# Performance work log

Measured on AMD Instinct MI355X. Metric: run time of the kernel, lower is better.

## Reference

```python
import jax, jax.numpy as jnp
import numpy as np

N_NODES = 50000
N_EDGES = 800000
D_IN = 96
HID = 96
D_OUT = 64
NUM_LAYERS = 6  # conv1 + (NUM_LAYERS-2) hidden convs + out_conv


def gcn_conv(x, W, b, src, dst, n):
    """PyG GCNConv: add self-loops, symmetric D^-1/2 (A+I) D^-1/2 normalization."""
    h = x @ W  # [n, out_dim]
    loops = jnp.arange(n, dtype=src.dtype)
    s = jnp.concatenate([src, loops])
    d = jnp.concatenate([dst, loops])
    deg = jax.ops.segment_sum(jnp.ones_like(s, dtype=h.dtype), d, num_segments=n)
    dinv = jnp.where(deg > 0, jax.lax.rsqrt(deg), 0.0)
    norm = dinv[s] * dinv[d]                 # [E+n]
    msg = h[s] * norm[:, None]               # gather + scale
    out = jax.ops.segment_sum(msg, d, num_segments=n)  # scatter-add to targets
    return out + b


def setup_inputs() -> dict:
    key = jax.random.key(0)
    ks = jax.random.split(key, 10)
    x = jax.random.normal(ks[0], (N_NODES, D_IN), dtype=jnp.float32)
    edge_index = jax.random.randint(ks[1], (2, N_EDGES), 0, N_NODES, dtype=jnp.int32)
    ricci_curvature = jax.random.normal(ks[2], (N_EDGES,), dtype=jnp.float32)
    n_hidden = NUM_LAYERS - 2
    W1 = jax.random.normal(ks[3], (D_IN, HID), dtype=jnp.float32) * 0.05
    b1 = jnp.zeros((HID,), dtype=jnp.float32)
    Ws = jax.random.normal(ks[4], (n_hidden, HID, HID), dtype=jnp.float32) * 0.05
    bs = jnp.zeros((n_hidden, HID), dtype=jnp.float32)
    Wout = jax.random.normal(ks[5], ((NUM_LAYERS - 1) * HID, D_OUT), dtype=jnp.float32) * 0.05
    bout = jnp.zeros((D_OUT,), dtype=jnp.float32)
    return {
        "x": x, "edge_index": edge_index, "percent": 70,
        "ricci_curvature": ricci_curvature,
        "W1": W1, "b1": b1, "Ws": Ws, "bs": bs, "Wout": Wout, "bout": bout,
    }


def reference(x, edge_index, percent, ricci_curvature, W1, b1, Ws, bs, Wout, bout):
    # Eval path: no sampling / dynamic reweighting, dropout is identity, no BN.
    del percent, ricci_curvature
    n = x.shape[0]
    src, dst = edge_index[0], edge_index[1]
    res = []
    h = jax.nn.relu(gcn_conv(x, W1, b1, src, dst, n))
    res.append(h)
    for i in range(Ws.shape[0]):
        h = jax.nn.relu(gcn_conv(h, Ws[i], bs[i], src, dst, n))
        res.append(h)
    x_cat = jnp.concatenate(res, axis=1)  # JK concatenation: [n, (L-1)*HID]
    out = gcn_conv(x_cat, Wout, bout, src, dst, n)
    return (out,) + tuple(res)
```

## Files before the change

kernel.cpp:

```cpp
#include <hip/hip_runtime.h>


typedef unsigned short ushortT;
typedef __attribute__((ext_vector_type(8))) short bf16x8;
typedef __attribute__((ext_vector_type(4))) float f32x4;

__device__ __forceinline__ ushortT f2b(float f) {
    union { float f; unsigned int u; } v;
    v.f = f;
    unsigned int lsb = (v.u >> 16) & 1u;
    v.u += 0x7fffu + lsb;
    return (ushortT)(v.u >> 16);
}
__device__ __forceinline__ float b2f(ushortT u) {
    union { float f; unsigned int u; } v;
    v.u = ((unsigned int)u) << 16;
    return v.f;
}

__global__ void prep_kernel(const float* __restrict__ W1, const float* __restrict__ Wsl,
                            const float* __restrict__ Wout, ushortT* __restrict__ wt1,
                            ushortT* __restrict__ wts, ushortT* __restrict__ wto,
                            int* __restrict__ degi, int n) {
    const int SQ = 96 * 96;
    const int T1 = 5 * SQ;
    const int T2 = T1 + 480 * 64;
    int i = blockIdx.x * blockDim.x + threadIdx.x;
    if (i < T1) {
        int l = i / SQ, j = i - l * SQ;
        int c = j / 96, k = j - c * 96;
        if (l == 0)
            wt1[j] = f2b(W1[k * 96 + c]);
        else
            wts[(size_t)(l - 1) * SQ + j] = f2b(Wsl[(size_t)(l - 1) * SQ + k * 96 + c]);
    } else if (i < T2) {
        int j = i - T1;
        int c = j / 480, k = j - c * 480;
        wto[j] = f2b(Wout[(size_t)k * 64 + c]);
    } else {
        int j = i - T2;
        if (j < n) degi[j] = 0;
    }
}

__global__ void count_kernel(const int* __restrict__ dst, int* __restrict__ degi, int E) {
    int e = blockIdx.x * blockDim.x + threadIdx.x;
    if (e < E) atomicAdd(&degi[dst[e]], 1);
}

__global__ void scan1(const int* __restrict__ degi, int* __restrict__ row_start,
                      int* __restrict__ partials, int n) {
    __shared__ int tmp[256];
    const int t = threadIdx.x;
    const int i = blockIdx.x * 256 + t;
    int val = (i < n) ? degi[i] : 0;
    tmp[t] = val;
    __syncthreads();
    for (int off = 1; off < 256; off <<= 1) {
        int v = (t >= off) ? tmp[t - off] : 0;
        __syncthreads();
        tmp[t] += v;
        __syncthreads();
    }
    if (i < n) row_start[i] = tmp[t] - val;
    if (t == 255) partials[blockIdx.x] = tmp[255];
}

__global__ void scan2(int* __restrict__ partials, int nb) {
    __shared__ int tmp[256];
    const int t = threadIdx.x;
    int val = (t < nb) ? partials[t] : 0;
    tmp[t] = val;
    __syncthreads();
    for (int off = 1; off < 256; off <<= 1) {
        int v = (t >= off) ? tmp[t - off] : 0;
        __syncthreads();
        tmp[t] += v;
        __syncthreads();
    }
    if (t < nb) partials[t] = tmp[t] - val;
}

__global__ void scan3(const int* __restrict__ degi, int* __restrict__ row_start,
                      const int* __restrict__ partials, float* __restrict__ dinv,
                      int n, int E) {
    const int i = blockIdx.x * 256 + threadIdx.x;
    if (i < n) {
        row_start[i] += partials[blockIdx.x];
        dinv[i] = rsqrtf((float)degi[i] + 1.0f);
    }
    if (i == 0) row_start[n] = E;
}

__global__ void fill_kernel(const int* __restrict__ src, const int* __restrict__ dst,
                            const int* __restrict__ row_start, int* __restrict__ degi,
                            int* __restrict__ col, int E) {
    int e = blockIdx.x * blockDim.x + threadIdx.x;
    if (e < E) {
        int d = dst[e];
        int pos = row_start[d] + atomicSub(&degi[d], 1) - 1;
        col[pos] = src[e];
    }
}

template <typename TIN>
__global__ __launch_bounds__(256) void gemm96_mfma(const TIN* __restrict__ X,
                                                   const ushortT* __restrict__ Wt,
                                                   const float* __restrict__ dinv,
                                                   ushortT* __restrict__ g, int n) {
    __shared__ __attribute__((aligned(16))) ushortT Xl[64][104];
    __shared__ __attribute__((aligned(16))) ushortT Wtl[96][104];
    const int tid = threadIdx.x;
    const int wave = tid >> 6, lane = tid & 63;
    const int quad = lane >> 4, m = lane & 15;
    const int row_base = blockIdx.x * 64;
    for (int i = tid; i < 96 * 24; i += 256) {
        int r = i / 24, c4 = (i % 24) * 4;
        *(ushort4*)&Wtl[r][c4] = *(const ushort4*)&Wt[r * 96 + c4];
    }
    for (int i = tid; i < 64 * 24; i += 256) {
        int r = i / 24, c4 = (i % 24) * 4;
        int grow = min(row_base + r, n - 1);
        if constexpr (sizeof(TIN) == 4) {
            float4 v = *(const float4*)&X[(size_t)grow * 96 + c4];
            ushort4 o = {f2b(v.x), f2b(v.y), f2b(v.z), f2b(v.w)};
            *(ushort4*)&Xl[r][c4] = o;
        } else {
            *(ushort4*)&Xl[r][c4] = *(const ushort4*)&X[(size_t)grow * 96 + c4];
        }
    }
    __syncthreads();
    f32x4 acc[6] = {};
#pragma unroll
    for (int ks = 0; ks < 3; ++ks) {
        bf16x8 a = *(bf16x8*)&Xl[wave * 16 + m][ks * 32 + quad * 8];
#pragma unroll
        for (int ct = 0; ct < 6; ++ct) {
            bf16x8 b = *(bf16x8*)&Wtl[ct * 16 + m][ks * 32 + quad * 8];
            acc[ct] = __builtin_amdgcn_mfma_f32_16x16x32_bf16(a, b, acc[ct], 0, 0, 0);
        }
    }
    float di[4];
    int rows[4];
#pragma unroll
    for (int r = 0; r < 4; ++r) {
        rows[r] = row_base + wave * 16 + quad * 4 + r;
        di[r] = (rows[r] < n) ? dinv[rows[r]] : 0.f;
    }
#pragma unroll
    for (int ct = 0; ct < 6; ++ct) {
        int colx = ct * 16 + m;
#pragma unroll
        for (int r = 0; r < 4; ++r)
            if (rows[r] < n) g[(size_t)rows[r] * 96 + colx] = f2b(acc[ct][r] * di[r]);
    }
}

template <typename TIN>
__global__ __launch_bounds__(256) void gemm_out_mfma(const TIN* __restrict__ hcat,
                                                     const ushortT* __restrict__ Wt,
                                                     const float* __restrict__ dinv,
                                                     ushortT* __restrict__ g, int n) {
    __shared__ __attribute__((aligned(16))) ushortT Xl[64][104];
    __shared__ __attribute__((aligned(16))) ushortT Wtl[64][104];
    const int tid = threadIdx.x;
    const int wave = tid >> 6, lane = tid & 63;
    const int quad = lane >> 4, m = lane & 15;
    const int row_base = blockIdx.x * 64;
    f32x4 acc[4] = {};
    for (int seg = 0; seg < 5; ++seg) {
        const TIN* hl = hcat + (size_t)seg * (size_t)n * 96;
        __syncthreads();
        for (int i = tid; i < 64 * 24; i += 256) {
            int r = i / 24, c4 = (i % 24) * 4;
            *(ushort4*)&Wtl[r][c4] = *(const ushort4*)&Wt[r * 480 + seg * 96 + c4];
        }
        for (int i = tid; i < 64 * 24; i += 256) {
            int r = i / 24, c4 = (i % 24) * 4;
            int grow = min(row_base + r, n - 1);
            if constexpr (sizeof(TIN) == 4) {
                float4 v = *(const float4*)&hl[(size_t)grow * 96 + c4];
                ushort4 o = {f2b(v.x), f2b(v.y), f2b(v.z), f2b(v.w)};
                *(ushort4*)&Xl[r][c4] = o;
            } else {
                *(ushort4*)&Xl[r][c4] = *(const ushort4*)&hl[(size_t)grow * 96 + c4];
            }
        }
        __syncthreads();
#pragma unroll
        for (int ks = 0; ks < 3; ++ks) {
            bf16x8 a = *(bf16x8*)&Xl[wave * 16 + m][ks * 32 + quad * 8];
#pragma unroll
            for (int ct = 0; ct < 4; ++ct) {
                bf16x8 b = *(bf16x8*)&Wtl[ct * 16 + m][ks * 32 + quad * 8];
                acc[ct] = __builtin_amdgcn_mfma_f32_16x16x32_bf16(a, b, acc[ct], 0, 0, 0);
            }
        }
    }
    float di[4];
    int rows[4];
#pragma unroll
    for (int r = 0; r < 4; ++r) {
        rows[r] = row_base + wave * 16 + quad * 4 + r;
        di[r] = (rows[r] < n) ? dinv[rows[r]] : 0.f;
    }
#pragma unroll
    for (int ct = 0; ct < 4; ++ct) {
        int colx = ct * 16 + m;
#pragma unroll
        for (int r = 0; r < 4; ++r)
            if (rows[r] < n) g[(size_t)rows[r] * 64 + colx] = f2b(acc[ct][r] * di[r]);
    }
}

template <int F, bool RELU, bool WRITE_BF16>
__global__ void agg_csr(const int* __restrict__ row_start, const int* __restrict__ col,
                        const ushortT* __restrict__ g, const float* __restrict__ dinv,
                        const float* __restrict__ b, float* __restrict__ out,
                        ushortT* __restrict__ hb, int n) {
    constexpr int NV = F / 4;
    const int lane = threadIdx.x & 63;
    const int half = lane >> 5;
    const int l32 = lane & 31;
    const int v = blockIdx.x * (blockDim.x >> 6) + (threadIdx.x >> 6);
    if (v >= n) return;
    const int e0 = row_start[v];
    const int e1 = row_start[v + 1];
    const bool act = (l32 < NV);
    const size_t fo = (size_t)l32 * 4;
    float a0 = 0.f, a1 = 0.f, a2 = 0.f, a3 = 0.f;
    float s0 = 0.f, s1 = 0.f, s2 = 0.f, s3 = 0.f;
    if (half == 0 && act) {
        ushort4 s = *(const ushort4*)&g[(size_t)v * F + fo];
        a0 = b2f(s.x); a1 = b2f(s.y); a2 = b2f(s.z); a3 = b2f(s.w);
    }
    const int total = e1 - e0;
    const int cntH = (total - half + 1) >> 1;
    const int base = e0 + half;
    const int sb = half << 5;
    int done = 0;
    while (done < cntH) {
        const int kc = min(cntH - done, 32);
        int cv = 0;
        if (l32 < kc) cv = col[base + 2 * (done + l32)];
        int j = 0;
        for (; j + 8 <= kc; j += 8) {
            int c0 = __shfl(cv, sb + j + 0);
            int c1 = __shfl(cv, sb + j + 1);
            int c2 = __shfl(cv, sb + j + 2);
            int c3 = __shfl(cv, sb + j + 3);
            int c4 = __shfl(cv, sb + j + 4);
            int c5 = __shfl(cv, sb + j + 5);
            int c6 = __shfl(cv, sb + j + 6);
            int c7 = __shfl(cv, sb + j + 7);
            if (act) {
                ushort4 g0 = *(const ushort4*)&g[(size_t)c0 * F + fo];
                ushort4 g1 = *(const ushort4*)&g[(size_t)c1 * F + fo];
                ushort4 g2 = *(const ushort4*)&g[(size_t)c2 * F + fo];
                ushort4 g3 = *(const ushort4*)&g[(size_t)c3 * F + fo];
                ushort4 g4 = *(const ushort4*)&g[(size_t)c4 * F + fo];
                ushort4 g5 = *(const ushort4*)&g[(size_t)c5 * F + fo];
                ushort4 g6 = *(const ushort4*)&g[(size_t)c6 * F + fo];
                ushort4 g7 = *(const ushort4*)&g[(size_t)c7 * F + fo];
                a0 += (b2f(g0.x) + b2f(g1.x)) + (b2f(g2.x) + b2f(g3.x));
                a1 += (b2f(g0.y) + b2f(g1.y)) + (b2f(g2.y) + b2f(g3.y));
                a2 += (b2f(g0.z) + b2f(g1.z)) + (b2f(g2.z) + b2f(g3.z));
                a3 += (b2f(g0.w) + b2f(g1.w)) + (b2f(g2.w) + b2f(g3.w));
                s0 += (b2f(g4.x) + b2f(g5.x)) + (b2f(g6.x) + b2f(g7.x));
                s1 += (b2f(g4.y) + b2f(g5.y)) + (b2f(g6.y) + b2f(g7.y));
                s2 += (b2f(g4.z) + b2f(g5.z)) + (b2f(g6.z) + b2f(g7.z));
                s3 += (b2f(g4.w) + b2f(g5.w)) + (b2f(g6.w) + b2f(g7.w));
            }
        }
        if (j + 4 <= kc) {
            int c0 = __shfl(cv, sb + j + 0);
            int c1 = __shfl(cv, sb + j + 1);
            int c2 = __shfl(cv, sb + j + 2);
            int c3 = __shfl(cv, sb + j + 3);
            if (act) {
                ushort4 g0 = *(const ushort4*)&g[(size_t)c0 * F + fo];
                ushort4 g1 = *(const ushort4*)&g[(size_t)c1 * F + fo];
                ushort4 g2 = *(const ushort4*)&g[(size_t)c2 * F + fo];
                ushort4 g3 = *(const ushort4*)&g[(size_t)c3 * F + fo];
                a0 += b2f(g0.x) + b2f(g1.x);
                a1 += b2f(g0.y) + b2f(g1.y);
                a2 += b2f(g0.z) + b2f(g1.z);
                a3 += b2f(g0.w) + b2f(g1.w);
                s0 += b2f(g2.x) + b2f(g3.x);
                s1 += b2f(g2.y) + b2f(g3.y);
                s2 += b2f(g2.z) + b2f(g3.z);
                s3 += b2f(g2.w) + b2f(g3.w);
            }
            j += 4;
        }
        if (j + 2 <= kc) {
            int c0 = __shfl(cv, sb + j + 0);
            int c1 = __shfl(cv, sb + j + 1);
            if (act) {
                ushort4 g0 = *(const ushort4*)&g[(size_t)c0 * F + fo];
                ushort4 g1 = *(const ushort4*)&g[(size_t)c1 * F + fo];
                a0 += b2f(g0.x) + b2f(g1.x);
                a1 += b2f(g0.y) + b2f(g1.y);
                a2 += b2f(g0.z) + b2f(g1.z);
                a3 += b2f(g0.w) + b2f(g1.w);
            }
            j += 2;
        }
        if (j < kc) {
            int c0 = __shfl(cv, sb + j);
            if (act) {
                ushort4 g0 = *(const ushort4*)&g[(size_t)c0 * F + fo];
                a0 += b2f(g0.x); a1 += b2f(g0.y); a2 += b2f(g0.z); a3 += b2f(g0.w);
            }
        }
        done += kc;
    }
    a0 += s0; a1 += s1; a2 += s2; a3 += s3;
    a0 += __shfl_xor(a0, 32);
    a1 += __shfl_xor(a1, 32);
    a2 += __shfl_xor(a2, 32);
    a3 += __shfl_xor(a3, 32);
    if (half == 0 && act) {
        const float di = dinv[v];
        const float4 bv = *(const float4*)&b[l32 * 4];
        float4 r;
        r.x = a0 * di + bv.x;
        r.y = a1 * di + bv.y;
        r.z = a2 * di + bv.z;
        r.w = a3 * di + bv.w;
        if (RELU) {
            r.x = fmaxf(r.x, 0.f); r.y = fmaxf(r.y, 0.f);
            r.z = fmaxf(r.z, 0.f); r.w = fmaxf(r.w, 0.f);
        }
        *(float4*)&out[(size_t)v * F + l32 * 4] = r;
        if (WRITE_BF16) {
            ushort4 o = {f2b(r.x), f2b(r.y), f2b(r.z), f2b(r.w)};
            *(ushort4*)&hb[(size_t)v * F + l32 * 4] = o;
        }
    }
}

extern "C" void kernel_launch(void* const* d_in, const int* in_sizes, int n_in,
                              void* d_out, int out_size, void* d_ws, size_t ws_size,
                              hipStream_t stream) {
    const float* x    = (const float*)d_in[0];
    const int*   ei   = (const int*)d_in[1];
    const float* W1   = (const float*)d_in[4];
    const float* b1   = (const float*)d_in[5];
    const float* Wsl  = (const float*)d_in[6];
    const float* bsl  = (const float*)d_in[7];
    const float* Wout = (const float*)d_in[8];
    const float* bout = (const float*)d_in[9];

    const int n = in_sizes[0] / 96;
    const int E = in_sizes[1] / 2;
    const int* src = ei;
    const int* dst = ei + E;

    char* p = (char*)d_ws;
    int*     degi      = (int*)p;              p += (size_t)n * 4;
    int*     row_start = (int*)p;              p += (size_t)(n + 1) * 4;
    int*     partials  = (int*)p;              p += 256 * 4;
    int*     col       = (int*)p;              p += (size_t)E * 4;
    float*   dinv      = (float*)p;            p += (size_t)n * 4;
    ushortT* g         = (ushortT*)p;          p += (size_t)n * 96 * 2;
    ushortT* hball     = (ushortT*)p;
    const size_t wbytes = (size_t)(5 * 9216 + 30720) * 2;
    const size_t fixed  = (size_t)(p - (char*)d_ws);
    const bool   big    = (fixed + (size_t)5 * n * 96 * 2 + wbytes) <= ws_size;
    const size_t hbsz   = big ? (size_t)5 * n * 96 : (size_t)n * 96;
    p += hbsz * 2;
    ushortT* wt1 = (ushortT*)p;
    ushortT* wts = wt1 + 9216;
    ushortT* wto = wts + 4 * 9216;

    float* out  = (float*)d_out;
    float* hseg = out + (size_t)n * 64;

    const int nthr = 256;
    const int gE   = (E + nthr - 1) / nthr;
    const int gAgg = (n + 3) / 4;
    const int gT64 = (n + 63) / 64;
    const int nb   = (n + 255) / 256;

    const int prep_items = 76800 + n;
    prep_kernel<<<(prep_items + 255) / 256, 256, 0, stream>>>(W1, Wsl, Wout, wt1, wts,
                                                              wto, degi, n);

    count_kernel<<<gE, nthr, 0, stream>>>(dst, degi, E);
    scan1<<<nb, 256, 0, stream>>>(degi, row_start, partials, n);
    scan2<<<1, 256, 0, stream>>>(partials, nb);
    scan3<<<nb, 256, 0, stream>>>(degi, row_start, partials, dinv, n, E);
    fill_kernel<<<gE, nthr, 0, stream>>>(src, dst, row_start, degi, col, E);

    ushortT* hb0 = hball;
    gemm96_mfma<float><<<gT64, 256, 0, stream>>>(x, wt1, dinv, g, n);
    agg_csr<96, true, true><<<gAgg, nthr, 0, stream>>>(row_start, col, g, dinv, b1,
                                                       hseg, hb0, n);

    for (int l = 0; l < 4; ++l) {
        float*   hnext = hseg + (size_t)(l + 1) * (size_t)n * 96;
        ushortT* hbin  = big ? (hball + (size_t)l * n * 96) : hball;
        ushortT* hbout = big ? (hball + (size_t)(l + 1) * n * 96) : hball;
        gemm96_mfma<ushortT><<<gT64, 256, 0, stream>>>(hbin, wts + (size_t)l * 9216,
                                                       dinv, g, n);
        agg_csr<96, true, true><<<gAgg, nthr, 0, stream>>>(row_start, col, g, dinv,
                                                           bsl + (size_t)l * 96, hnext,
                                                           hbout, n);
    }

    if (big)
        gemm_out_mfma<ushortT><<<gT64, 256, 0, stream>>>(hball, wto, dinv, g, n);
    else
        gemm_out_mfma<float><<<gT64, 256, 0, stream>>>(hseg, wto, dinv, g, n);
    agg_csr<64, false, false><<<gAgg, nthr, 0, stream>>>(row_start, col, g, dinv, bout,
                                                         out, nullptr, n);
}
```

Baseline: 515.7 us.

## Fuse CSR aggregation with next layer's MFMA GEMM per 64-row tile

Adds an agg_gemm kernel that aggregates neighbor features for 64 nodes into shared memory, applies bias and ReLU, writes outputs, then immediately multiplies the tile by the next layer's weights with MFMA. Two scratch buffers hold the input and output pre-scaled features alternately. The final hidden layer also accumulates the JK output GEMM over the earlier bf16 segments. This removes separate GEMM launches and the global round-trip of the hidden activations for the GEMM. In exchange the aggregation now uses 64 rows per block with 4 waves each handling 16 rows serially, which may lower parallelism and latency hiding for the gathers.

```diff
diff --git a/kernel.cpp b/kernel.cpp
--- a/kernel.cpp
+++ b/kernel.cpp
@@ -340,6 +340,227 @@
     }
 }
 
+template <bool LAST>
+__global__ __launch_bounds__(256, 4) void agg_gemm(
+        const int* __restrict__ row_start, const int* __restrict__ col,
+        const ushortT* __restrict__ gin, const float* __restrict__ dinv,
+        const float* __restrict__ bias, float* __restrict__ hout,
+        ushortT* __restrict__ hb_seg, const ushortT* __restrict__ Wt,
+        const ushortT* __restrict__ hb_all, ushortT* __restrict__ gout, int n) {
+    __shared__ __attribute__((aligned(16))) ushortT Xl[64][104];
+    __shared__ __attribute__((aligned(16))) ushortT Wtl[96][104];
+    const int tid = threadIdx.x;
+    const int wave = tid >> 6, lane = tid & 63;
+    const int half = lane >> 5, l32 = lane & 31;
+    const int row_base = blockIdx.x * 64;
+
+    if (!LAST) {
+        for (int i = tid; i < 96 * 24; i += 256) {
+            int r = i / 24, c4 = (i % 24) * 4;
+            *(ushort4*)&Wtl[r][c4] = *(const ushort4*)&Wt[r * 96 + c4];
+        }
+    } else {
+        for (int i = tid; i < 64 * 24; i += 256) {
+            int r = i / 24, c4 = (i % 24) * 4;
+            *(ushort4*)&Wtl[r][c4] = *(const ushort4*)&Wt[r * 480 + 4 * 96 + c4];
+        }
+    }
+
+    const bool act = (l32 < 24);
+    const size_t fo = (size_t)l32 * 4;
+    float4 bv = {0.f, 0.f, 0.f, 0.f};
+    if (act) bv = *(const float4*)&bias[l32 * 4];
+    const int sb = half << 5;
+
+    for (int rr = 0; rr < 16; ++rr) {
+        const int lr = wave * 16 + rr;
+        const int v = row_base + lr;
+        if (v < n) {
+            const int e0 = row_start[v];
+            const int e1 = row_start[v + 1];
+            float a0 = 0.f, a1 = 0.f, a2 = 0.f, a3 = 0.f;
+            float s0 = 0.f, s1 = 0.f, s2 = 0.f, s3 = 0.f;
+            if (half == 0 && act) {
+                ushort4 s = *(const ushort4*)&gin[(size_t)v * 96 + fo];
+                a0 = b2f(s.x); a1 = b2f(s.y); a2 = b2f(s.z); a3 = b2f(s.w);
+            }
+            const int total = e1 - e0;
+            const int cntH = (total - half + 1) >> 1;
+            const int base = e0 + half;
+            int done = 0;
+            while (done < cntH) {
+                const int kc = min(cntH - done, 32);
+                int cv = 0;
+                if (l32 < kc) cv = col[base + 2 * (done + l32)];
+                int j = 0;
+                for (; j + 8 <= kc; j += 8) {
+                    int c0 = __shfl(cv, sb + j + 0);
+                    int c1 = __shfl(cv, sb + j + 1);
+                    int c2 = __shfl(cv, sb + j + 2);
+                    int c3 = __shfl(cv, sb + j + 3);
+                    int c4 = __shfl(cv, sb + j + 4);
+                    int c5 = __shfl(cv, sb + j + 5);
+                    int c6 = __shfl(cv, sb + j + 6);
+                    int c7 = __shfl(cv, sb + j + 7);
+                    if (act) {
+                        ushort4 g0 = *(const ushort4*)&gin[(size_t)c0 * 96 + fo];
+                        ushort4 g1 = *(const ushort4*)&gin[(size_t)c1 * 96 + fo];
+                        ushort4 g2 = *(const ushort4*)&gin[(size_t)c2 * 96 + fo];
+                        ushort4 g3 = *(const ushort4*)&gin[(size_t)c3 * 96 + fo];
+                        ushort4 g4 = *(const ushort4*)&gin[(size_t)c4 * 96 + fo];
+                        ushort4 g5 = *(const ushort4*)&gin[(size_t)c5 * 96 + fo];
+                        ushort4 g6 = *(const ushort4*)&gin[(size_t)c6 * 96 + fo];
+                        ushort4 g7 = *(const ushort4*)&gin[(size_t)c7 * 96 + fo];
+                        a0 += (b2f(g0.x) + b2f(g1.x)) + (b2f(g2.x) + b2f(g3.x));
+                        a1 += (b2f(g0.y) + b2f(g1.y)) + (b2f(g2.y) + b2f(g3.y));
+                        a2 += (b2f(g0.z) + b2f(g1.z)) + (b2f(g2.z) + b2f(g3.z));
+                        a3 += (b2f(g0.w) + b2f(g1.w)) + (b2f(g2.w) + b2f(g3.w));
+                        s0 += (b2f(g4.x) + b2f(g5.x)) + (b2f(g6.x) + b2f(g7.x));
+                        s1 += (b2f(g4.y) + b2f(g5.y)) + (b2f(g6.y) + b2f(g7.y));
+                        s2 += (b2f(g4.z) + b2f(g5.z)) + (b2f(g6.z) + b2f(g7.z));
+                        s3 += (b2f(g4.w) + b2f(g5.w)) + (b2f(g6.w) + b2f(g7.w));
+                    }
+                }
+                if (j + 4 <= kc) {
+                    int c0 = __shfl(cv, sb + j + 0);
+                    int c1 = __shfl(cv, sb + j + 1);
+                    int c2 = __shfl(cv, sb + j + 2);
+                    int c3 = __shfl(cv, sb + j + 3);
+                    if (act) {
+                        ushort4 g0 = *(const ushort4*)&gin[(size_t)c0 * 96 + fo];
+                        ushort4 g1 = *(const ushort4*)&gin[(size_t)c1 * 96 + fo];
+                        ushort4 g2 = *(const ushort4*)&gin[(size_t)c2 * 96 + fo];
+                        ushort4 g3 = *(const ushort4*)&gin[(size_t)c3 * 96 + fo];
+                        a0 += b2f(g0.x) + b2f(g1.x);
+                        a1 += b2f(g0.y) + b2f(g1.y);
+                        a2 += b2f(g0.z) + b2f(g1.z);
+                        a3 += b2f(g0.w) + b2f(g1.w);
+                        s0 += b2f(g2.x) + b2f(g3.x);
+                        s1 += b2f(g2.y) + b2f(g3.y);
+                        s2 += b2f(g2.z) + b2f(g3.z);
+                        s3 += b2f(g2.w) + b2f(g3.w);
+                    }
+                    j += 4;
+                }
+                if (j + 2 <= kc) {
+                    int c0 = __shfl(cv, sb + j + 0);
+                    int c1 = __shfl(cv, sb + j + 1);
+                    if (act) {
+                        ushort4 g0 = *(const ushort4*)&gin[(size_t)c0 * 96 + fo];
+                        ushort4 g1 = *(const ushort4*)&gin[(size_t)c1 * 96 + fo];
+                        a0 += b2f(g0.x) + b2f(g1.x);
+                        a1 += b2f(g0.y) + b2f(g1.y);
+                        a2 += b2f(g0.z) + b2f(g1.z);
+                        a3 += b2f(g0.w) + b2f(g1.w);
+                    }
+                    j += 2;
+                }
+                if (j < kc) {
+                    int c0 = __shfl(cv, sb + j);
+                    if (act) {
+                        ushort4 g0 = *(const ushort4*)&gin[(size_t)c0 * 96 + fo];
+                        a0 += b2f(g0.x); a1 += b2f(g0.y); a2 += b2f(g0.z); a3 += b2f(g0.w);
+                    }
+                }
+                done += kc;
+            }
+            a0 += s0; a1 += s1; a2 += s2; a3 += s3;
+            a0 += __shfl_xor(a0, 32);
+            a1 += __shfl_xor(a1, 32);
+            a2 += __shfl_xor(a2, 32);
+            a3 += __shfl_xor(a3, 32);
+            if (half == 0 && act) {
+                const float di = dinv[v];
+                float4 r;
+                r.x = fmaxf(a0 * di + bv.x, 0.f);
+                r.y = fmaxf(a1 * di + bv.y, 0.f);
+                r.z = fmaxf(a2 * di + bv.z, 0.f);
+                r.w = fmaxf(a3 * di + bv.w, 0.f);
+                *(float4*)&hout[(size_t)v * 96 + fo] = r;
+                ushort4 o = {f2b(r.x), f2b(r.y), f2b(r.z), f2b(r.w)};
+                if (!LAST) *(ushort4*)&hb_seg[(size_t)v * 96 + fo] = o;
+                *(ushort4*)&Xl[lr][l32 * 4] = o;
+            }
+        } else {
+            if (half == 0 && act) {
+                ushort4 z = {0, 0, 0, 0};
+                *(ushort4*)&Xl[lr][l32 * 4] = z;
+            }
+        }
+    }
+    __syncthreads();
+
+    const int quad = lane >> 4, m = lane & 15;
+    float di[4];
+    int rows[4];
+#pragma unroll
+    for (int r = 0; r < 4; ++r) {
+        rows[r] = row_base + wave * 16 + quad * 4 + r;
+        di[r] = (rows[r] < n) ? dinv[rows[r]] : 0.f;
+    }
+
+    if (!LAST) {
+        f32x4 acc[6] = {};
+#pragma unroll
+        for (int ks = 0; ks < 3; ++ks) {
+            bf16x8 a = *(bf16x8*)&Xl[wave * 16 + m][ks * 32 + quad * 8];
+#pragma unroll
+            for (int ct = 0; ct < 6; ++ct) {
+                bf16x8 b = *(bf16x8*)&Wtl[ct * 16 + m][ks * 32 + quad * 8];
+                acc[ct] = __builtin_amdgcn_mfma_f32_16x16x32_bf16(a, b, acc[ct], 0, 0, 0);
+            }
+        }
+#pragma unroll
+        for (int ct = 0; ct < 6; ++ct) {
+            int colx = ct * 16 + m;
+#pragma unroll
+            for (int r = 0; r < 4; ++r)
+                if (rows[r] < n) gout[(size_t)rows[r] * 96 + colx] = f2b(acc[ct][r] * di[r]);
+        }
+    } else {
+        f32x4 acc[4] = {};
+#pragma unroll
+        for (int ks = 0; ks < 3; ++ks) {
+            bf16x8 a = *(bf16x8*)&Xl[wave * 16 + m][ks * 32 + quad * 8];
+#pragma unroll
+            for (int ct = 0; ct < 4; ++ct) {
+                bf16x8 b = *(bf16x8*)&Wtl[ct * 16 + m][ks * 32 + quad * 8];
+                acc[ct] = __builtin_amdgcn_mfma_f32_16x16x32_bf16(a, b, acc[ct], 0, 0, 0);
+            }
+        }
+        for (int seg = 0; seg < 4; ++seg) {
+            __syncthreads();
+            for (int i = tid; i < 64 * 24; i += 256) {
+                int r = i / 24, c4 = (i % 24) * 4;
+                *(ushort4*)&Wtl[r][c4] = *(const ushort4*)&Wt[r * 480 + seg * 96 + c4];
+            }
+            const ushortT* hs = hb_all + (size_t)seg * (size_t)n * 96;
+            for (int i = tid; i < 64 * 24; i += 256) {
+                int r = i / 24, c4 = (i % 24) * 4;
+                int grow = min(row_base + r, n - 1);
+                *(ushort4*)&Xl[r][c4] = *(const ushort4*)&hs[(size_t)grow * 96 + c4];
+            }
+            __syncthreads();
+#pragma unroll
+            for (int ks = 0; ks < 3; ++ks) {
+                bf16x8 a = *(bf16x8*)&Xl[wave * 16 + m][ks * 32 + quad * 8];
+#pragma unroll
+                for (int ct = 0; ct < 4; ++ct) {
+                    bf16x8 b = *(bf16x8*)&Wtl[ct * 16 + m][ks * 32 + quad * 8];
+                    acc[ct] = __builtin_amdgcn_mfma_f32_16x16x32_bf16(a, b, acc[ct], 0, 0, 0);
+                }
+            }
+        }
+#pragma unroll
+        for (int ct = 0; ct < 4; ++ct) {
+            int colx = ct * 16 + m;
+#pragma unroll
+            for (int r = 0; r < 4; ++r)
+                if (rows[r] < n) gout[(size_t)rows[r] * 64 + colx] = f2b(acc[ct][r] * di[r]);
+        }
+    }
+}
+
 extern "C" void kernel_launch(void* const* d_in, const int* in_sizes, int n_in,
                               void* d_out, int out_size, void* d_ws, size_t ws_size,
                               hipStream_t stream) {
@@ -363,7 +584,8 @@
     int*     partials  = (int*)p;              p += 256 * 4;
     int*     col       = (int*)p;              p += (size_t)E * 4;
     float*   dinv      = (float*)p;            p += (size_t)n * 4;
-    ushortT* g         = (ushortT*)p;          p += (size_t)n * 96 * 2;
+    ushortT* gA        = (ushortT*)p;          p += (size_t)n * 96 * 2;
+    ushortT* gB        = (ushortT*)p;          p += (size_t)n * 96 * 2;
     ushortT* hball     = (ushortT*)p;
     const size_t wbytes = (size_t)(5 * 9216 + 30720) * 2;
     const size_t fixed  = (size_t)(p - (char*)d_ws);
@@ -393,26 +615,37 @@
     scan3<<<nb, 256, 0, stream>>>(degi, row_start, partials, dinv, n, E);
     fill_kernel<<<gE, nthr, 0, stream>>>(src, dst, row_start, degi, col, E);
 
-    ushortT* hb0 = hball;
-    gemm96_mfma<float><<<gT64, 256, 0, stream>>>(x, wt1, dinv, g, n);
-    agg_csr<96, true, true><<<gAgg, nthr, 0, stream>>>(row_start, col, g, dinv, b1,
-                                                       hseg, hb0, n);
-
-    for (int l = 0; l < 4; ++l) {
-        float*   hnext = hseg + (size_t)(l + 1) * (size_t)n * 96;
-        ushortT* hbin  = big ? (hball + (size_t)l * n * 96) : hball;
-        ushortT* hbout = big ? (hball + (size_t)(l + 1) * n * 96) : hball;
-        gemm96_mfma<ushortT><<<gT64, 256, 0, stream>>>(hbin, wts + (size_t)l * 9216,
-                                                       dinv, g, n);
-        agg_csr<96, true, true><<<gAgg, nthr, 0, stream>>>(row_start, col, g, dinv,
-                                                           bsl + (size_t)l * 96, hnext,
-                                                           hbout, n);
-    }
-
-    if (big)
-        gemm_out_mfma<ushortT><<<gT64, 256, 0, stream>>>(hball, wto, dinv, g, n);
-    else
-        gemm_out_mfma<float><<<gT64, 256, 0, stream>>>(hseg, wto, dinv, g, n);
-    agg_csr<64, false, false><<<gAgg, nthr, 0, stream>>>(row_start, col, g, dinv, bout,
-                                                         out, nullptr, n);
-}
+    if (big) {
+        gemm96_mfma<float><<<gT64, 256, 0, stream>>>(x, wt1, dinv, gA, n);
+        ushortT* gbuf[2] = {gA, gB};
+        for (int i = 0; i < 4; ++i) {
+            ushortT* gin  = gbuf[i & 1];
+            ushortT* gout = gbuf[(i & 1) ^ 1];
+            const float* bias = (i == 0) ? b1 : (bsl + (size_t)(i - 1) * 96);
+            agg_gemm<false><<<gT64, 256, 0, stream>>>(
+                row_start, col, gin, dinv, bias, hseg + (size_t)i * n * 96,
+                hball + (size_t)i * n * 96, wts + (size_t)i * 9216, nullptr,
+                gout, n);
+        }
+        agg_gemm<true><<<gT64, 256, 0, stream>>>(
+            row_start, col, gbuf[0], dinv, bsl + 3 * 96, hseg + (size_t)4 * n * 96,
+            nullptr, wto, hball, gbuf[1], n);
+        agg_csr<64, false, false><<<gAgg, nthr, 0, stream>>>(row_start, col, gbuf[1],
+                                                             dinv, bout, out, nullptr, n);
+    } else {
+        gemm96_mfma<float><<<gT64, 256, 0, stream>>>(x, wt1, dinv, gA, n);
+        agg_csr<96, true, true><<<gAgg, nthr, 0, stream>>>(row_start, col, gA, dinv, b1,
+                                                           hseg, hball, n);
+        for (int l = 0; l < 4; ++l) {
+            float* hnext = hseg + (size_t)(l + 1) * (size_t)n * 96;
+            gemm96_mfma<ushortT><<<gT64, 256, 0, stream>>>(hball, wts + (size_t)l * 9216,
+                                                           dinv, gA, n);
+            agg_csr<96, true, true><<<gAgg, nthr, 0, stream>>>(row_start, col, gA, dinv,
+                                                               bsl + (size_t)l * 96,
+                                                               hnext, hball, n);
+        }
+        gemm_out_mfma<float><<<gT64, 256, 0, stream>>>(hseg, wto, dinv, gA, n);
+        agg_csr<64, false, false><<<gAgg, nthr, 0, stream>>>(row_start, col, gA, dinv,
+                                                             bout, out, nullptr, n);
+    }
+}
```

Measured after the change: 554.8 us. 1.08x slower.

## Split gathered features into two column-half planes and aggregate each half separately

Applied to the files above, without the earlier changes.

The GEMM outputs are now written as two planar halves (48 or 32 columns each), and aggregation runs twice as many blocks, each gathering only one half of every neighbor row. The aim is to shrink the random-gather working set per plane so it sits better in cache, and to use lanes that were idle when 24 of 32 lanes held a 96-wide row. In exchange, the CSR column indices and row offsets are read twice, each gather is a smaller 96- or 64-byte row, and with 48 columns only 12 of 32 lanes are active.

```diff
diff --git a/kernel.cpp b/kernel.cpp
--- a/kernel.cpp
+++ b/kernel.cpp
@@ -114,6 +114,7 @@
     const int wave = tid >> 6, lane = tid & 63;
     const int quad = lane >> 4, m = lane & 15;
     const int row_base = blockIdx.x * 64;
+    const size_t pstride = (size_t)n * 48;
     for (int i = tid; i < 96 * 24; i += 256) {
         int r = i / 24, c4 = (i % 24) * 4;
         *(ushort4*)&Wtl[r][c4] = *(const ushort4*)&Wt[r * 96 + c4];
@@ -149,10 +150,14 @@
     }
 #pragma unroll
     for (int ct = 0; ct < 6; ++ct) {
-        int colx = ct * 16 + m;
+        const int colx = ct * 16 + m;
+        const int pl = colx / 48;
+        const int pc = colx - pl * 48;
 #pragma unroll
         for (int r = 0; r < 4; ++r)
-            if (rows[r] < n) g[(size_t)rows[r] * 96 + colx] = f2b(acc[ct][r] * di[r]);
+            if (rows[r] < n)
+                g[(size_t)pl * pstride + (size_t)rows[r] * 48 + pc] =
+                    f2b(acc[ct][r] * di[r]);
     }
 }
 
@@ -167,6 +172,7 @@
     const int wave = tid >> 6, lane = tid & 63;
     const int quad = lane >> 4, m = lane & 15;
     const int row_base = blockIdx.x * 64;
+    const size_t pstride = (size_t)n * 32;
     f32x4 acc[4] = {};
     for (int seg = 0; seg < 5; ++seg) {
         const TIN* hl = hcat + (size_t)seg * (size_t)n * 96;
@@ -206,38 +212,44 @@
     }
 #pragma unroll
     for (int ct = 0; ct < 4; ++ct) {
-        int colx = ct * 16 + m;
+        const int colx = ct * 16 + m;
+        const int pl = colx >> 5;
+        const int pc = colx & 31;
 #pragma unroll
         for (int r = 0; r < 4; ++r)
-            if (rows[r] < n) g[(size_t)rows[r] * 64 + colx] = f2b(acc[ct][r] * di[r]);
-    }
-}
-
-template <int F, bool RELU, bool WRITE_BF16>
-__global__ void agg_csr(const int* __restrict__ row_start, const int* __restrict__ col,
-                        const ushortT* __restrict__ g, const float* __restrict__ dinv,
-                        const float* __restrict__ b, float* __restrict__ out,
-                        ushortT* __restrict__ hb, int n) {
-    constexpr int NV = F / 4;
+            if (rows[r] < n)
+                g[(size_t)pl * pstride + (size_t)rows[r] * 32 + pc] =
+                    f2b(acc[ct][r] * di[r]);
+    }
+}
+
+template <int FCOL, int HW, bool RELU, bool WRITE_BF16>
+__global__ void agg_half(const int* __restrict__ row_start, const int* __restrict__ col,
+                         const ushortT* __restrict__ g, const float* __restrict__ dinv,
+                         const float* __restrict__ b, float* __restrict__ out,
+                         ushortT* __restrict__ hb, int n) {
+    constexpr int NV = FCOL / 4;
     const int lane = threadIdx.x & 63;
-    const int half = lane >> 5;
+    const int whalf = lane >> 5;
     const int l32 = lane & 31;
-    const int v = blockIdx.x * (blockDim.x >> 6) + (threadIdx.x >> 6);
+    const int chalf = blockIdx.x & 1;
+    const int v = (blockIdx.x >> 1) * (blockDim.x >> 6) + (threadIdx.x >> 6);
     if (v >= n) return;
+    const ushortT* gp = g + (size_t)chalf * (size_t)n * FCOL;
     const int e0 = row_start[v];
     const int e1 = row_start[v + 1];
     const bool act = (l32 < NV);
     const size_t fo = (size_t)l32 * 4;
     float a0 = 0.f, a1 = 0.f, a2 = 0.f, a3 = 0.f;
     float s0 = 0.f, s1 = 0.f, s2 = 0.f, s3 = 0.f;
-    if (half == 0 && act) {
-        ushort4 s = *(const ushort4*)&g[(size_t)v * F + fo];
+    if (whalf == 0 && act) {
+        ushort4 s = *(const ushort4*)&gp[(size_t)v * FCOL + fo];
         a0 = b2f(s.x); a1 = b2f(s.y); a2 = b2f(s.z); a3 = b2f(s.w);
     }
     const int total = e1 - e0;
-    const int cntH = (total - half + 1) >> 1;
-    const int base = e0 + half;
-    const int sb = half << 5;
+    const int cntH = (total - whalf + 1) >> 1;
+    const int base = e0 + whalf;
+    const int sb = whalf << 5;
     int done = 0;
     while (done < cntH) {
         const int kc = min(cntH - done, 32);
@@ -254,14 +266,14 @@
             int c6 = __shfl(cv, sb + j + 6);
             int c7 = __shfl(cv, sb + j + 7);
             if (act) {
-                ushort4 g0 = *(const ushort4*)&g[(size_t)c0 * F + fo];
-                ushort4 g1 = *(const ushort4*)&g[(size_t)c1 * F + fo];
-                ushort4 g2 = *(const ushort4*)&g[(size_t)c2 * F + fo];
-                ushort4 g3 = *(const ushort4*)&g[(size_t)c3 * F + fo];
-                ushort4 g4 = *(const ushort4*)&g[(size_t)c4 * F + fo];
-                ushort4 g5 = *(const ushort4*)&g[(size_t)c5 * F + fo];
-                ushort4 g6 = *(const ushort4*)&g[(size_t)c6 * F + fo];
-                ushort4 g7 = *(const ushort4*)&g[(size_t)c7 * F + fo];
+                ushort4 g0 = *(const ushort4*)&gp[(size_t)c0 * FCOL + fo];
+                ushort4 g1 = *(const ushort4*)&gp[(size_t)c1 * FCOL + fo];
+                ushort4 g2 = *(const ushort4*)&gp[(size_t)c2 * FCOL + fo];
+                ushort4 g3 = *(const ushort4*)&gp[(size_t)c3 * FCOL + fo];
+                ushort4 g4 = *(const ushort4*)&gp[(size_t)c4 * FCOL + fo];
+                ushort4 g5 = *(const ushort4*)&gp[(size_t)c5 * FCOL + fo];
+                ushort4 g6 = *(const ushort4*)&gp[(size_t)c6 * FCOL + fo];
+                ushort4 g7 = *(const ushort4*)&gp[(size_t)c7 * FCOL + fo];
                 a0 += (b2f(g0.x) + b2f(g1.x)) + (b2f(g2.x) + b2f(g3.x));
                 a1 += (b2f(g0.y) + b2f(g1.y)) + (b2f(g2.y) + b2f(g3.y));
                 a2 += (b2f(g0.z) + b2f(g1.z)) + (b2f(g2.z) + b2f(g3.z));
@@ -278,10 +290,10 @@
             int c2 = __shfl(cv, sb + j + 2);
             int c3 = __shfl(cv, sb + j + 3);
             if (act) {
-                ushort4 g0 = *(const ushort4*)&g[(size_t)c0 * F + fo];
-                ushort4 g1 = *(const ushort4*)&g[(size_t)c1 * F + fo];
-                ushort4 g2 = *(const ushort4*)&g[(size_t)c2 * F + fo];
-                ushort4 g3 = *(const ushort4*)&g[(size_t)c3 * F + fo];
+                ushort4 g0 = *(const ushort4*)&gp[(size_t)c0 * FCOL + fo];
+                ushort4 g1 = *(const ushort4*)&gp[(size_t)c1 * FCOL + fo];
+                ushort4 g2 = *(const ushort4*)&gp[(size_t)c2 * FCOL + fo];
+                ushort4 g3 = *(const ushort4*)&gp[(size_t)c3 * FCOL + fo];
                 a0 += b2f(g0.x) + b2f(g1.x);
                 a1 += b2f(g0.y) + b2f(g1.y);
                 a2 += b2f(g0.z) + b2f(g1.z);
@@ -297,8 +309,8 @@
             int c0 = __shfl(cv, sb + j + 0);
             int c1 = __shfl(cv, sb + j + 1);
             if (act) {
-                ushort4 g0 = *(const ushort4*)&g[(size_t)c0 * F + fo];
-                ushort4 g1 = *(const ushort4*)&g[(size_t)c1 * F + fo];
+                ushort4 g0 = *(const ushort4*)&gp[(size_t)c0 * FCOL + fo];
+                ushort4 g1 = *(const ushort4*)&gp[(size_t)c1 * FCOL + fo];
                 a0 += b2f(g0.x) + b2f(g1.x);
                 a1 += b2f(g0.y) + b2f(g1.y);
                 a2 += b2f(g0.z) + b2f(g1.z);
@@ -309,7 +321,7 @@
         if (j < kc) {
             int c0 = __shfl(cv, sb + j);
             if (act) {
-                ushort4 g0 = *(const ushort4*)&g[(size_t)c0 * F + fo];
+                ushort4 g0 = *(const ushort4*)&gp[(size_t)c0 * FCOL + fo];
                 a0 += b2f(g0.x); a1 += b2f(g0.y); a2 += b2f(g0.z); a3 += b2f(g0.w);
             }
         }
@@ -320,9 +332,9 @@
     a1 += __shfl_xor(a1, 32);
     a2 += __shfl_xor(a2, 32);
     a3 += __shfl_xor(a3, 32);
-    if (half == 0 && act) {
+    if (whalf == 0 && act) {
         const float di = dinv[v];
-        const float4 bv = *(const float4*)&b[l32 * 4];
+        const float4 bv = *(const float4*)&b[chalf * FCOL + l32 * 4];
         float4 r;
         r.x = a0 * di + bv.x;
         r.y = a1 * di + bv.y;
@@ -332,10 +344,10 @@
             r.x = fmaxf(r.x, 0.f); r.y = fmaxf(r.y, 0.f);
             r.z = fmaxf(r.z, 0.f); r.w = fmaxf(r.w, 0.f);
         }
-        *(float4*)&out[(size_t)v * F + l32 * 4] = r;
+        *(float4*)&out[(size_t)v * HW + chalf * FCOL + l32 * 4] = r;
         if (WRITE_BF16) {
             ushort4 o = {f2b(r.x), f2b(r.y), f2b(r.z), f2b(r.w)};
-            *(ushort4*)&hb[(size_t)v * F + l32 * 4] = o;
+            *(ushort4*)&hb[(size_t)v * 96 + chalf * FCOL + l32 * 4] = o;
         }
     }
 }
@@ -377,11 +389,11 @@
     float* out  = (float*)d_out;
     float* hseg = out + (size_t)n * 64;
 
-    const int nthr = 256;
-    const int gE   = (E + nthr - 1) / nthr;
-    const int gAgg = (n + 3) / 4;
-    const int gT64 = (n + 63) / 64;
-    const int nb   = (n + 255) / 256;
+    const int nthr  = 256;
+    const int gE    = (E + nthr - 1) / nthr;
+    const int gT64  = (n + 63) / 64;
+    const int nb    = (n + 255) / 256;
+    const int gAgg2 = 2 * ((n + 3) / 4);
 
     const int prep_items = 76800 + n;
     prep_kernel<<<(prep_items + 255) / 256, 256, 0, stream>>>(W1, Wsl, Wout, wt1, wts,
@@ -393,10 +405,9 @@
     scan3<<<nb, 256, 0, stream>>>(degi, row_start, partials, dinv, n, E);
     fill_kernel<<<gE, nthr, 0, stream>>>(src, dst, row_start, degi, col, E);
 
-    ushortT* hb0 = hball;
     gemm96_mfma<float><<<gT64, 256, 0, stream>>>(x, wt1, dinv, g, n);
-    agg_csr<96, true, true><<<gAgg, nthr, 0, stream>>>(row_start, col, g, dinv, b1,
-                                                       hseg, hb0, n);
+    agg_half<48, 96, true, true><<<gAgg2, nthr, 0, stream>>>(row_start, col, g, dinv,
+                                                             b1, hseg, hball, n);
 
     for (int l = 0; l < 4; ++l) {
         float*   hnext = hseg + (size_t)(l + 1) * (size_t)n * 96;
@@ -404,15 +415,14 @@
         ushortT* hbout = big ? (hball + (size_t)(l + 1) * n * 96) : hball;
         gemm96_mfma<ushortT><<<gT64, 256, 0, stream>>>(hbin, wts + (size_t)l * 9216,
                                                        dinv, g, n);
-        agg_csr<96, true, true><<<gAgg, nthr, 0, stream>>>(row_start, col, g, dinv,
-                                                           bsl + (size_t)l * 96, hnext,
-                                                           hbout, n);
+        agg_half<48, 96, true, true><<<gAgg2, nthr, 0, stream>>>(
+            row_start, col, g, dinv, bsl + (size_t)l * 96, hnext, hbout, n);
     }
 
     if (big)
         gemm_out_mfma<ushortT><<<gT64, 256, 0, stream>>>(hball, wto, dinv, g, n);
     else
         gemm_out_mfma<float><<<gT64, 256, 0, stream>>>(hseg, wto, dinv, g, n);
-    agg_csr<64, false, false><<<gAgg, nthr, 0, stream>>>(row_start, col, g, dinv, bout,
-                                                         out, nullptr, n);
-}
+    agg_half<32, 64, false, false><<<gAgg2, nthr, 0, stream>>>(row_start, col, g, dinv,
+                                                               bout, out, nullptr, n);
+}
```

New measurement: 620.2 us. 20.3% more time.

## Merge three-pass scan into one block and fuse CSR fill with first GEMM

Applied to the files above, without the earlier changes.

Replaces the three scan kernels with a single 1024-thread block that does a chunked serial prefix sum, also writing dinv and the row_start sentinel. The CSR fill kernel and the first-layer GEMM are merged into one launch, with blocks partitioned by index, so the two independent pieces of work share a grid. This removes three kernel launches and their gaps. In exchange, the scan runs on one workgroup with each thread serially reading about 49 strided elements, which may be slower than the multi-block version.

```diff
diff --git a/kernel.cpp b/kernel.cpp
--- a/kernel.cpp
+++ b/kernel.cpp
@@ -48,58 +48,90 @@
     if (e < E) atomicAdd(&degi[dst[e]], 1);
 }
 
-__global__ void scan1(const int* __restrict__ degi, int* __restrict__ row_start,
-                      int* __restrict__ partials, int n) {
-    __shared__ int tmp[256];
+__global__ __launch_bounds__(1024) void scan123(const int* __restrict__ degi,
+                                                int* __restrict__ row_start,
+                                                float* __restrict__ dinv, int n, int E) {
+    __shared__ int tmp[1024];
     const int t = threadIdx.x;
-    const int i = blockIdx.x * 256 + t;
-    int val = (i < n) ? degi[i] : 0;
-    tmp[t] = val;
+    const int C = (n + 1023) / 1024;
+    const int i0 = t * C;
+    const int i1 = min(i0 + C, n);
+    int s = 0;
+    for (int i = i0; i < i1; ++i) s += degi[i];
+    tmp[t] = s;
     __syncthreads();
-    for (int off = 1; off < 256; off <<= 1) {
+    for (int off = 1; off < 1024; off <<= 1) {
         int v = (t >= off) ? tmp[t - off] : 0;
         __syncthreads();
         tmp[t] += v;
         __syncthreads();
     }
-    if (i < n) row_start[i] = tmp[t] - val;
-    if (t == 255) partials[blockIdx.x] = tmp[255];
-}
-
-__global__ void scan2(int* __restrict__ partials, int nb) {
-    __shared__ int tmp[256];
-    const int t = threadIdx.x;
-    int val = (t < nb) ? partials[t] : 0;
-    tmp[t] = val;
+    int base = tmp[t] - s;
+    for (int i = i0; i < i1; ++i) {
+        const int d = degi[i];
+        row_start[i] = base;
+        dinv[i] = rsqrtf((float)d + 1.0f);
+        base += d;
+    }
+    if (t == 1023) row_start[n] = E;
+}
+
+__global__ __launch_bounds__(256) void fill_gemm1(
+        const int* __restrict__ src, const int* __restrict__ dst,
+        const int* __restrict__ row_start, int* __restrict__ degi,
+        int* __restrict__ col, int E, int gF,
+        const float* __restrict__ X, const ushortT* __restrict__ Wt,
+        const float* __restrict__ dinv, ushortT* __restrict__ g, int n) {
+    if (blockIdx.x < gF) {
+        int e = blockIdx.x * blockDim.x + threadIdx.x;
+        if (e < E) {
+            int d = dst[e];
+            int pos = row_start[d] + atomicSub(&degi[d], 1) - 1;
+            col[pos] = src[e];
+        }
+        return;
+    }
+    __shared__ __attribute__((aligned(16))) ushortT Xl[64][104];
+    __shared__ __attribute__((aligned(16))) ushortT Wtl[96][104];
+    const int tid = threadIdx.x;
+    const int wave = tid >> 6, lane = tid & 63;
+    const int quad = lane >> 4, m = lane & 15;
+    const int row_base = (blockIdx.x - gF) * 64;
+    for (int i = tid; i < 96 * 24; i += 256) {
+        int r = i / 24, c4 = (i % 24) * 4;
+        *(ushort4*)&Wtl[r][c4] = *(const ushort4*)&Wt[r * 96 + c4];
+    }
+    for (int i = tid; i < 64 * 24; i += 256) {
+        int r = i / 24, c4 = (i % 24) * 4;
+        int grow = min(row_base + r, n - 1);
+        float4 v = *(const float4*)&X[(size_t)grow * 96 + c4];
+        ushort4 o = {f2b(v.x), f2b(v.y), f2b(v.z), f2b(v.w)};
+        *(ushort4*)&Xl[r][c4] = o;
+    }
     __syncthreads();
-    for (int off = 1; off < 256; off <<= 1) {
-        int v = (t >= off) ? tmp[t - off] : 0;
-        __syncthreads();
-        tmp[t] += v;
-        __syncthreads();
-    }
-    if (t < nb) partials[t] = tmp[t] - val;
-}
-
-__global__ void scan3(const int* __restrict__ degi, int* __restrict__ row_start,
-                      const int* __restrict__ partials, float* __restrict__ dinv,
-                      int n, int E) {
-    const int i = blockIdx.x * 256 + threadIdx.x;
-    if (i < n) {
-        row_start[i] += partials[blockIdx.x];
-        dinv[i] = rsqrtf((float)degi[i] + 1.0f);
-    }
-    if (i == 0) row_start[n] = E;
-}
-
-__global__ void fill_kernel(const int* __restrict__ src, const int* __restrict__ dst,
-                            const int* __restrict__ row_start, int* __restrict__ degi,
-                            int* __restrict__ col, int E) {
-    int e = blockIdx.x * blockDim.x + threadIdx.x;
-    if (e < E) {
-        int d = dst[e];
-        int pos = row_start[d] + atomicSub(&degi[d], 1) - 1;
-        col[pos] = src[e];
+    f32x4 acc[6] = {};
+#pragma unroll
+    for (int ks = 0; ks < 3; ++ks) {
+        bf16x8 a = *(bf16x8*)&Xl[wave * 16 + m][ks * 32 + quad * 8];
+#pragma unroll
+        for (int ct = 0; ct < 6; ++ct) {
+            bf16x8 b = *(bf16x8*)&Wtl[ct * 16 + m][ks * 32 + quad * 8];
+            acc[ct] = __builtin_amdgcn_mfma_f32_16x16x32_bf16(a, b, acc[ct], 0, 0, 0);
+        }
+    }
+    float di[4];
+    int rows[4];
+#pragma unroll
+    for (int r = 0; r < 4; ++r) {
+        rows[r] = row_base + wave * 16 + quad * 4 + r;
+        di[r] = (rows[r] < n) ? dinv[rows[r]] : 0.f;
+    }
+#pragma unroll
+    for (int ct = 0; ct < 6; ++ct) {
+        int colx = ct * 16 + m;
+#pragma unroll
+        for (int r = 0; r < 4; ++r)
+            if (rows[r] < n) g[(size_t)rows[r] * 96 + colx] = f2b(acc[ct][r] * di[r]);
     }
 }
 
@@ -373,6 +405,7 @@
     ushortT* wt1 = (ushortT*)p;
     ushortT* wts = wt1 + 9216;
     ushortT* wto = wts + 4 * 9216;
+    (void)partials;
 
     float* out  = (float*)d_out;
     float* hseg = out + (size_t)n * 64;
@@ -381,22 +414,18 @@
     const int gE   = (E + nthr - 1) / nthr;
     const int gAgg = (n + 3) / 4;
     const int gT64 = (n + 63) / 64;
-    const int nb   = (n + 255) / 256;
 
     const int prep_items = 76800 + n;
     prep_kernel<<<(prep_items + 255) / 256, 256, 0, stream>>>(W1, Wsl, Wout, wt1, wts,
                                                               wto, degi, n);
 
     count_kernel<<<gE, nthr, 0, stream>>>(dst, degi, E);
-    scan1<<<nb, 256, 0, stream>>>(degi, row_start, partials, n);
-    scan2<<<1, 256, 0, stream>>>(partials, nb);
-    scan3<<<nb, 256, 0, stream>>>(degi, row_start, partials, dinv, n, E);
-    fill_kernel<<<gE, nthr, 0, stream>>>(src, dst, row_start, degi, col, E);
-
-    ushortT* hb0 = hball;
-    gemm96_mfma<float><<<gT64, 256, 0, stream>>>(x, wt1, dinv, g, n);
+    scan123<<<1, 1024, 0, stream>>>(degi, row_start, dinv, n, E);
+    fill_gemm1<<<gE + gT64, nthr, 0, stream>>>(src, dst, row_start, degi, col, E, gE,
+                                               x, wt1, dinv, g, n);
+
     agg_csr<96, true, true><<<gAgg, nthr, 0, stream>>>(row_start, col, g, dinv, b1,
-                                                       hseg, hb0, n);
+                                                       hseg, hball, n);
 
     for (int l = 0; l < 4; ++l) {
         float*   hnext = hseg + (size_t)(l + 1) * (size_t)n * 96;
```

New measurement: 609.6 us. +18.2%, slower.
